# Kernel tuning notes

Hardware: AMD Instinct MI355X
Metric: run time of the kernel (lower is better)

The kernel has to match this reference:

```python
import jax, jax.numpy as jnp
import numpy as np

T, H, I, E, K = 1024, 2048, 1408, 8, 2  # tokens, hidden, moe_intermediate, n_experts, top_k

def setup_inputs() -> dict:
    key = jax.random.key(0)
    k0, k1, k2, k3 = jax.random.split(key, 4)
    def w(k, shape, fan_in):
        return jax.random.normal(k, shape, jnp.float32) / np.float32(np.sqrt(fan_in))
    return {
        "hidden_states": jax.random.normal(k0, (T, H), jnp.float32),
        "gate_w": w(k1, (H, E), H),      # router: LiteLinear(H -> E), no bias
        "w1": w(k2, (E, H, I), H),        # experts_w1 [E, H, I]
        "w2": w(k3, (E, I, H), I),        # experts_w2 [E, I, H]
    }

def reference(hidden_states, gate_w, w1, w2):
    # Router: logits -> softmax -> top-k expert probabilities (no renorm; Qwen2MoE norm_topk_prob=False)
    router_logits = hidden_states @ gate_w                      # [T, E]
    probs = jax.nn.softmax(router_logits, axis=-1)              # [T, E]
    topk_vals, topk_idx = jax.lax.top_k(probs, K)               # [T, K]
    # Dense combine weights: zero except at the top-k experts of each token
    combine = jnp.sum(jax.nn.one_hot(topk_idx, E, dtype=probs.dtype) * topk_vals[..., None], axis=1)  # [T, E]
    # Expert MLP per source: down(silu(x @ w1)) — note: no gate/up split in this repo's fused_moe weights
    h = jnp.einsum('th,ehi->tei', hidden_states, w1)            # [T, E, I]
    y = jnp.einsum('tei,eih->teh', jax.nn.silu(h), w2)          # [T, E, H]
    return jnp.einsum('te,teh->th', combine, y)                 # [T, H]
```

## Files before the change

### kernel.cpp

```cpp
#include <hip/hip_runtime.h>
#include <hip/hip_fp16.h>

#define T_TOK 1024
#define H_DIM 2048
#define I_DIM 1408
#define N_EXP 8
#define TOPK  2

using f16x8 = __attribute__((ext_vector_type(8))) _Float16;
using f32x4 = __attribute__((ext_vector_type(4))) float;

#define BM 64
#define BN 64
#define BK 64
#define NTHR 256
#define MBLKS 32

#define WS_COUNTS      0
#define WS_BASES       256
#define WS_CURSORS     512
#define WS_TOPK_E      768
#define WS_TOPK_W      (768 + 8192)
#define WS_TOK_OF_SLOT 17408
#define WS_W_OF_SLOT   29696
#define WS_HACT        43008
#define WS_NEEDED      (43008 + 8650752)

__global__ void k_router(const float* __restrict__ X, const float* __restrict__ GW,
                         int* __restrict__ counts, int* __restrict__ topk_e,
                         float* __restrict__ topk_w) {
    int t = (blockIdx.x * blockDim.x + threadIdx.x) >> 6;
    int lane = threadIdx.x & 63;
    if (t >= T_TOK) return;
    float acc[N_EXP];
#pragma unroll
    for (int e = 0; e < N_EXP; ++e) acc[e] = 0.f;
    const float* xrow = X + (size_t)t * H_DIM;
    for (int h = lane; h < H_DIM; h += 64) {
        float x = xrow[h];
        const float* g = GW + (size_t)h * N_EXP;
#pragma unroll
        for (int e = 0; e < N_EXP; ++e) acc[e] = fmaf(x, g[e], acc[e]);
    }
#pragma unroll
    for (int off = 32; off > 0; off >>= 1) {
#pragma unroll
        for (int e = 0; e < N_EXP; ++e) acc[e] += __shfl_xor(acc[e], off, 64);
    }
    if (lane == 0) {
        float m = acc[0];
#pragma unroll
        for (int e = 1; e < N_EXP; ++e) m = fmaxf(m, acc[e]);
        float ex[N_EXP], s = 0.f;
#pragma unroll
        for (int e = 0; e < N_EXP; ++e) { ex[e] = expf(acc[e] - m); s += ex[e]; }
        float inv = 1.f / s;
        int e1 = 0;
#pragma unroll
        for (int e = 1; e < N_EXP; ++e) if (ex[e] > ex[e1]) e1 = e;
        int e2 = (e1 == 0) ? 1 : 0;
#pragma unroll
        for (int e = 0; e < N_EXP; ++e) if (e != e1 && ex[e] > ex[e2]) e2 = e;
        topk_e[t * 2 + 0] = e1;
        topk_e[t * 2 + 1] = e2;
        topk_w[t * 2 + 0] = ex[e1] * inv;
        topk_w[t * 2 + 1] = ex[e2] * inv;
        atomicAdd(&counts[e1], 1);
        atomicAdd(&counts[e2], 1);
    }
}

__global__ void k_prefix(const int* __restrict__ counts, int* __restrict__ bases,
                         int* __restrict__ cursors) {
    if (threadIdx.x == 0) {
        int b = 0;
        for (int e = 0; e < N_EXP; ++e) {
            bases[e] = b;
            b += ((counts[e] + BM - 1) / BM) * BM;
            cursors[e] = 0;
        }
    }
}

__global__ void k_scatter(const int* __restrict__ topk_e, const float* __restrict__ topk_w,
                          const int* __restrict__ bases, int* __restrict__ cursors,
                          int* __restrict__ tok_of_slot, float* __restrict__ w_of_slot) {
    int t = blockIdx.x * blockDim.x + threadIdx.x;
    if (t >= T_TOK) return;
    for (int j = 0; j < TOPK; ++j) {
        int e = topk_e[t * 2 + j];
        int pos = atomicAdd(&cursors[e], 1);
        int slot = bases[e] + pos;
        tok_of_slot[slot] = t;
        w_of_slot[slot] = topk_w[t * 2 + j];
    }
}


#define G_COMPUTE(buf)                                                          \
    do {                                                                        \
        _Pragma("unroll") for (int ks = 0; ks < 2; ++ks) {                      \
            f16x8 af[2], bf[2];                                                 \
            _Pragma("unroll") for (int ii = 0; ii < 2; ++ii) {                  \
                int r = wm + ii * 16 + rsel;                                    \
                af[ii] = *(const f16x8*)&As[buf][r][((kq + 4 * ks) ^ (r & 7)) * 8]; \
            }                                                                   \
            _Pragma("unroll") for (int jj = 0; jj < 2; ++jj) {                  \
                int r = wn + jj * 16 + rsel;                                    \
                bf[jj] = *(const f16x8*)&Bs[buf][r][((kq + 4 * ks) ^ (r & 7)) * 8]; \
            }                                                                   \
            _Pragma("unroll") for (int ii = 0; ii < 2; ++ii)                    \
                _Pragma("unroll") for (int jj = 0; jj < 2; ++jj)                \
                    acc[ii][jj] = __builtin_amdgcn_mfma_f32_16x16x32_f16(af[ii], bf[jj], acc[ii][jj], 0, 0, 0); \
        }                                                                       \
    } while (0)

#define G_DECODE(NB)                                \
    const int bi = blockIdx.x;                      \
    const int xcd = bi & 7;                         \
    const int kk = bi >> 3;                         \
    const int mblk = kk & (MBLKS - 1);              \
    const int P = xcd + 8 * (kk >> 5);              \
    const int e = P / (NB);                         \
    const int n = P % (NB);

__global__ __launch_bounds__(NTHR, 3) void k_gemm1(
    const float* __restrict__ X, const float* __restrict__ W1,
    const int* __restrict__ counts, const int* __restrict__ bases,
    const int* __restrict__ tok_of_slot, const float* __restrict__ w_of_slot,
    _Float16* __restrict__ hact) {
    __shared__ _Float16 As[2][BM][BK];
    __shared__ _Float16 Bs[2][BN][BK];

    G_DECODE(I_DIM / BN)
    const int cnt = counts[e];
    const int m0 = mblk * BM;
    if (m0 >= cnt) return;
    const int base = bases[e];
    const int n0 = n * BN;
    const int tid = threadIdx.x;

    const int ar = tid >> 2;
    const int as0 = (tid & 3) * 2;
    const int r_eff = min(ar, cnt - m0 - 1);
    const float* arow = X + (size_t)tok_of_slot[base + m0 + r_eff] * H_DIM + (tid & 3) * 16;

    const int bn = tid & 63;
    const int bc2 = (tid >> 6) * 2;
    const float* bcol = W1 + (size_t)e * (H_DIM * I_DIM) + (size_t)(bc2 * 8) * I_DIM + n0 + bn;

    const int wid = tid >> 6, lane = tid & 63;
    const int wm = (wid >> 1) * 32, wn = (wid & 1) * 32;
    const int rsel = lane & 15, kq = lane >> 4;

    f32x4 acc[2][2] = {};

    float4 aS0[4], aS1[4];
    float  bS0[16], bS1[16];

#define G1_LOAD(aS, bS, k0)                                        \
    do {                                                           \
        const float* ap = arow + (k0);                             \
        aS[0] = *(const float4*)(ap);                              \
        aS[1] = *(const float4*)(ap + 4);                          \
        aS[2] = *(const float4*)(ap + 8);                          \
        aS[3] = *(const float4*)(ap + 12);                         \
        const float* bp = bcol + (size_t)(k0) * I_DIM;             \
        _Pragma("unroll") for (int j = 0; j < 16; ++j)             \
            bS[j] = bp[(size_t)j * I_DIM];                         \
    } while (0)

#define G1_STORE(buf, aS, bS)                                      \
    do {                                                           \
        f16x8 p0, p1;                                              \
        _Pragma("unroll") for (int c = 0; c < 4; ++c) {            \
            p0[c] = (_Float16)aS[0][c]; p0[c + 4] = (_Float16)aS[1][c]; \
            p1[c] = (_Float16)aS[2][c]; p1[c + 4] = (_Float16)aS[3][c]; \
        }                                                          \
        *(f16x8*)&As[buf][ar][((as0) ^ (ar & 7)) * 8] = p0;        \
        *(f16x8*)&As[buf][ar][((as0 + 1) ^ (ar & 7)) * 8] = p1;    \
        f16x8 q0, q1;                                              \
        _Pragma("unroll") for (int j = 0; j < 8; ++j) {            \
            q0[j] = (_Float16)bS[j]; q1[j] = (_Float16)bS[j + 8];  \
        }                                                          \
        *(f16x8*)&Bs[buf][bn][((bc2) ^ (bn & 7)) * 8] = q0;        \
        *(f16x8*)&Bs[buf][bn][((bc2 + 1) ^ (bn & 7)) * 8] = q1;    \
    } while (0)

    constexpr int KT = H_DIM / BK;
    G1_LOAD(aS0, bS0, 0);
    G1_STORE(0, aS0, bS0);
    G1_LOAD(aS0, bS0, BK);
    __syncthreads();
    for (int kt = 0; kt < KT; kt += 2) {
        if (kt + 2 < KT) G1_LOAD(aS1, bS1, (kt + 2) * BK);
        G_COMPUTE(0);
        if (kt + 1 < KT) G1_STORE(1, aS0, bS0);
        __syncthreads();
        if (kt + 3 < KT) G1_LOAD(aS0, bS0, (kt + 3) * BK);
        if (kt + 1 < KT) {
            G_COMPUTE(1);
            if (kt + 2 < KT) G1_STORE(0, aS1, bS1);
            __syncthreads();
        }
    }
#undef G1_LOAD
#undef G1_STORE

    const int rows = cnt - m0;
#pragma unroll
    for (int i = 0; i < 2; ++i) {
#pragma unroll
        for (int rg = 0; rg < 4; ++rg) {
            int r = wm + i * 16 + kq * 4 + rg;
            if (r < rows) {
                int slot = base + m0 + r;
                float w = w_of_slot[slot];
                _Float16* hrow = hact + (size_t)slot * I_DIM + n0;
#pragma unroll
                for (int j = 0; j < 2; ++j) {
                    float v = acc[i][j][rg];
                    hrow[wn + j * 16 + rsel] = (_Float16)(v / (1.f + expf(-v)) * w);
                }
            }
        }
    }
}

__global__ __launch_bounds__(NTHR, 3) void k_gemm2(
    const _Float16* __restrict__ hact, const float* __restrict__ W2,
    const int* __restrict__ counts, const int* __restrict__ bases,
    const int* __restrict__ tok_of_slot, float* __restrict__ out) {
    __shared__ _Float16 As[2][BM][BK];
    __shared__ _Float16 Bs[2][BN][BK];

    G_DECODE(H_DIM / BN)
    const int cnt = counts[e];
    const int m0 = mblk * BM;
    if (m0 >= cnt) return;
    const int base = bases[e];
    const int n0 = n * BN;
    const int tid = threadIdx.x;

    const int ar = tid >> 2;
    const int as0 = (tid & 3) * 2;
    const int r_eff = min(ar, cnt - m0 - 1);
    const _Float16* arow = hact + (size_t)(base + m0 + r_eff) * I_DIM + (tid & 3) * 16;

    const int bn = tid & 63;
    const int bc2 = (tid >> 6) * 2;
    const float* bcol = W2 + (size_t)e * (I_DIM * H_DIM) + (size_t)(bc2 * 8) * H_DIM + n0 + bn;

    const int wid = tid >> 6, lane = tid & 63;
    const int wm = (wid >> 1) * 32, wn = (wid & 1) * 32;
    const int rsel = lane & 15, kq = lane >> 4;

    f32x4 acc[2][2] = {};

    f16x8 aS0[2], aS1[2];
    float bS0[16], bS1[16];

#define G2_LOAD(aS, bS, k0)                                        \
    do {                                                           \
        const _Float16* ap = arow + (k0);                          \
        aS[0] = *(const f16x8*)(ap);                               \
        aS[1] = *(const f16x8*)(ap + 8);                           \
        const float* bp = bcol + (size_t)(k0) * H_DIM;             \
        _Pragma("unroll") for (int j = 0; j < 16; ++j)             \
            bS[j] = bp[(size_t)j * H_DIM];                         \
    } while (0)

#define G2_STORE(buf, aS, bS)                                      \
    do {                                                           \
        *(f16x8*)&As[buf][ar][((as0) ^ (ar & 7)) * 8] = aS[0];     \
        *(f16x8*)&As[buf][ar][((as0 + 1) ^ (ar & 7)) * 8] = aS[1]; \
        f16x8 q0, q1;                                              \
        _Pragma("unroll") for (int j = 0; j < 8; ++j) {            \
            q0[j] = (_Float16)bS[j]; q1[j] = (_Float16)bS[j + 8];  \
        }                                                          \
        *(f16x8*)&Bs[buf][bn][((bc2) ^ (bn & 7)) * 8] = q0;        \
        *(f16x8*)&Bs[buf][bn][((bc2 + 1) ^ (bn & 7)) * 8] = q1;    \
    } while (0)

    constexpr int KT = I_DIM / BK;
    G2_LOAD(aS0, bS0, 0);
    G2_STORE(0, aS0, bS0);
    G2_LOAD(aS0, bS0, BK);
    __syncthreads();
    for (int kt = 0; kt < KT; kt += 2) {
        if (kt + 2 < KT) G2_LOAD(aS1, bS1, (kt + 2) * BK);
        G_COMPUTE(0);
        if (kt + 1 < KT) G2_STORE(1, aS0, bS0);
        __syncthreads();
        if (kt + 3 < KT) G2_LOAD(aS0, bS0, (kt + 3) * BK);
        if (kt + 1 < KT) {
            G_COMPUTE(1);
            if (kt + 2 < KT) G2_STORE(0, aS1, bS1);
            __syncthreads();
        }
    }
#undef G2_LOAD
#undef G2_STORE

    const int rows = cnt - m0;
#pragma unroll
    for (int i = 0; i < 2; ++i) {
#pragma unroll
        for (int rg = 0; rg < 4; ++rg) {
            int r = wm + i * 16 + kq * 4 + rg;
            if (r < rows) {
                int slot = base + m0 + r;
                int tok = tok_of_slot[slot];
                float* orow = out + (size_t)tok * H_DIM + n0;
#pragma unroll
                for (int j = 0; j < 2; ++j)
                    atomicAdd(&orow[wn + j * 16 + rsel], acc[i][j][rg]);
            }
        }
    }
}

extern "C" void kernel_launch(void* const* d_in, const int* in_sizes, int n_in,
                              void* d_out, int out_size, void* d_ws, size_t ws_size,
                              hipStream_t stream) {
    const float* X  = (const float*)d_in[0];
    const float* GW = (const float*)d_in[1];
    const float* W1 = (const float*)d_in[2];
    const float* W2 = (const float*)d_in[3];
    float* out = (float*)d_out;
    char* ws = (char*)d_ws;
    if (ws_size < (size_t)WS_NEEDED) return;

    int*   counts      = (int*)(ws + WS_COUNTS);
    int*   bases       = (int*)(ws + WS_BASES);
    int*   cursors     = (int*)(ws + WS_CURSORS);
    int*   topk_e      = (int*)(ws + WS_TOPK_E);
    float* topk_w      = (float*)(ws + WS_TOPK_W);
    int*   tok_of_slot = (int*)(ws + WS_TOK_OF_SLOT);
    float* w_of_slot   = (float*)(ws + WS_W_OF_SLOT);
    _Float16* hact     = (_Float16*)(ws + WS_HACT);

    hipMemsetAsync(counts, 0, N_EXP * sizeof(int), stream);
    k_router<<<T_TOK / 4, 256, 0, stream>>>(X, GW, counts, topk_e, topk_w);
    k_prefix<<<1, 64, 0, stream>>>(counts, bases, cursors);
    k_scatter<<<T_TOK / 256, 256, 0, stream>>>(topk_e, topk_w, bases, cursors,
                                               tok_of_slot, w_of_slot);
    hipMemsetAsync(out, 0, (size_t)T_TOK * H_DIM * sizeof(float), stream);
    k_gemm1<<<8 * MBLKS * 22, NTHR, 0, stream>>>(
        X, W1, counts, bases, tok_of_slot, w_of_slot, hact);
    k_gemm2<<<8 * MBLKS * 32, NTHR, 0, stream>>>(
        hact, W2, counts, bases, tok_of_slot, out);
}
```

Measured before the change: 184.5 us.

## Deepen global-load register prefetch to four stages in both expert GEMMs

Both expert GEMM kernels now keep four K-tiles of global loads in flight in registers instead of two, rotating through four register buffers while still double-buffering shared memory. Scheduling barriers keep the compiler from interleaving the compute and store phases, and launch bounds drop from 3 to 2 blocks per SM to make room for the extra registers. The aim is to hide the latency of the strided fp32 weight loads, at the cost of lower occupancy and higher register pressure.

```diff
diff --git a/kernel.cpp b/kernel.cpp
--- a/kernel.cpp
+++ b/kernel.cpp
@@ -15,6 +15,8 @@
 #define BK 64
 #define NTHR 256
 #define MBLKS 32
+
+#define SB() __builtin_amdgcn_sched_barrier(0)
 
 #define WS_COUNTS      0
 #define WS_BASES       256
@@ -124,7 +126,7 @@
     const int e = P / (NB);                         \
     const int n = P % (NB);
 
-__global__ __launch_bounds__(NTHR, 3) void k_gemm1(
+__global__ __launch_bounds__(NTHR, 2) void k_gemm1(
     const float* __restrict__ X, const float* __restrict__ W1,
     const int* __restrict__ counts, const int* __restrict__ bases,
     const int* __restrict__ tok_of_slot, const float* __restrict__ w_of_slot,
@@ -155,17 +157,17 @@
 
     f32x4 acc[2][2] = {};
 
-    float4 aS0[4], aS1[4];
-    float  bS0[16], bS1[16];
-
-#define G1_LOAD(aS, bS, k0)                                        \
+    float aS0[16], aS1[16], aS2[16], aS3[16];
+    float bS0[16], bS1[16], bS2[16], bS3[16];
+
+#define G1_LOAD(aS, bS, t)                                         \
     do {                                                           \
-        const float* ap = arow + (k0);                             \
-        aS[0] = *(const float4*)(ap);                              \
-        aS[1] = *(const float4*)(ap + 4);                          \
-        aS[2] = *(const float4*)(ap + 8);                          \
-        aS[3] = *(const float4*)(ap + 12);                         \
-        const float* bp = bcol + (size_t)(k0) * I_DIM;             \
+        const float* ap = arow + (t) * BK;                         \
+        *(float4*)(aS + 0)  = *(const float4*)(ap);                \
+        *(float4*)(aS + 4)  = *(const float4*)(ap + 4);            \
+        *(float4*)(aS + 8)  = *(const float4*)(ap + 8);            \
+        *(float4*)(aS + 12) = *(const float4*)(ap + 12);           \
+        const float* bp = bcol + (size_t)((t) * BK) * I_DIM;       \
         _Pragma("unroll") for (int j = 0; j < 16; ++j)             \
             bS[j] = bp[(size_t)j * I_DIM];                         \
     } while (0)
@@ -173,9 +175,8 @@
 #define G1_STORE(buf, aS, bS)                                      \
     do {                                                           \
         f16x8 p0, p1;                                              \
-        _Pragma("unroll") for (int c = 0; c < 4; ++c) {            \
-            p0[c] = (_Float16)aS[0][c]; p0[c + 4] = (_Float16)aS[1][c]; \
-            p1[c] = (_Float16)aS[2][c]; p1[c + 4] = (_Float16)aS[3][c]; \
+        _Pragma("unroll") for (int c = 0; c < 8; ++c) {            \
+            p0[c] = (_Float16)aS[c]; p1[c] = (_Float16)aS[c + 8];  \
         }                                                          \
         *(f16x8*)&As[buf][ar][((as0) ^ (ar & 7)) * 8] = p0;        \
         *(f16x8*)&As[buf][ar][((as0 + 1) ^ (ar & 7)) * 8] = p1;    \
@@ -188,22 +189,31 @@
     } while (0)
 
     constexpr int KT = H_DIM / BK;
+    constexpr int QUADS = (KT - 1) / 4;
+    constexpr int REM = (KT - 1) & 3;
+
     G1_LOAD(aS0, bS0, 0);
+    G1_LOAD(aS1, bS1, 1);
+    G1_LOAD(aS2, bS2, 2);
+    G1_LOAD(aS3, bS3, 3);
     G1_STORE(0, aS0, bS0);
-    G1_LOAD(aS0, bS0, BK);
     __syncthreads();
-    for (int kt = 0; kt < KT; kt += 2) {
-        if (kt + 2 < KT) G1_LOAD(aS1, bS1, (kt + 2) * BK);
-        G_COMPUTE(0);
-        if (kt + 1 < KT) G1_STORE(1, aS0, bS0);
-        __syncthreads();
-        if (kt + 3 < KT) G1_LOAD(aS0, bS0, (kt + 3) * BK);
-        if (kt + 1 < KT) {
-            G_COMPUTE(1);
-            if (kt + 2 < KT) G1_STORE(0, aS1, bS1);
-            __syncthreads();
-        }
-    }
+
+    int h = 0;
+    for (int q = 0; q < QUADS; ++q, h += 4) {
+        if (h + 4 < KT) G1_LOAD(aS0, bS0, h + 4);
+        SB(); G_COMPUTE(0); SB(); G1_STORE(1, aS1, bS1); __syncthreads();
+        if (h + 5 < KT) G1_LOAD(aS1, bS1, h + 5);
+        SB(); G_COMPUTE(1); SB(); G1_STORE(0, aS2, bS2); __syncthreads();
+        if (h + 6 < KT) G1_LOAD(aS2, bS2, h + 6);
+        SB(); G_COMPUTE(0); SB(); G1_STORE(1, aS3, bS3); __syncthreads();
+        if (h + 7 < KT) G1_LOAD(aS3, bS3, h + 7);
+        SB(); G_COMPUTE(1); SB(); G1_STORE(0, aS0, bS0); __syncthreads();
+    }
+    if constexpr (REM >= 1) { G_COMPUTE(0); G1_STORE(1, aS1, bS1); __syncthreads(); }
+    if constexpr (REM >= 2) { G_COMPUTE(1); G1_STORE(0, aS2, bS2); __syncthreads(); }
+    if constexpr (REM >= 3) { G_COMPUTE(0); G1_STORE(1, aS3, bS3); __syncthreads(); }
+    G_COMPUTE((KT - 1) & 1);
 #undef G1_LOAD
 #undef G1_STORE
 
@@ -227,7 +237,7 @@
     }
 }
 
-__global__ __launch_bounds__(NTHR, 3) void k_gemm2(
+__global__ __launch_bounds__(NTHR, 2) void k_gemm2(
     const _Float16* __restrict__ hact, const float* __restrict__ W2,
     const int* __restrict__ counts, const int* __restrict__ bases,
     const int* __restrict__ tok_of_slot, float* __restrict__ out) {
@@ -257,15 +267,15 @@
 
     f32x4 acc[2][2] = {};
 
-    f16x8 aS0[2], aS1[2];
-    float bS0[16], bS1[16];
-
-#define G2_LOAD(aS, bS, k0)                                        \
+    f16x8 aS0[2], aS1[2], aS2[2], aS3[2];
+    float bS0[16], bS1[16], bS2[16], bS3[16];
+
+#define G2_LOAD(aS, bS, t)                                         \
     do {                                                           \
-        const _Float16* ap = arow + (k0);                          \
+        const _Float16* ap = arow + (t) * BK;                      \
         aS[0] = *(const f16x8*)(ap);                               \
         aS[1] = *(const f16x8*)(ap + 8);                           \
-        const float* bp = bcol + (size_t)(k0) * H_DIM;             \
+        const float* bp = bcol + (size_t)((t) * BK) * H_DIM;       \
         _Pragma("unroll") for (int j = 0; j < 16; ++j)             \
             bS[j] = bp[(size_t)j * H_DIM];                         \
     } while (0)
@@ -283,22 +293,31 @@
     } while (0)
 
     constexpr int KT = I_DIM / BK;
+    constexpr int QUADS = (KT - 1) / 4;
+    constexpr int REM = (KT - 1) & 3;
+
     G2_LOAD(aS0, bS0, 0);
+    G2_LOAD(aS1, bS1, 1);
+    G2_LOAD(aS2, bS2, 2);
+    G2_LOAD(aS3, bS3, 3);
     G2_STORE(0, aS0, bS0);
-    G2_LOAD(aS0, bS0, BK);
     __syncthreads();
-    for (int kt = 0; kt < KT; kt += 2) {
-        if (kt + 2 < KT) G2_LOAD(aS1, bS1, (kt + 2) * BK);
-        G_COMPUTE(0);
-        if (kt + 1 < KT) G2_STORE(1, aS0, bS0);
-        __syncthreads();
-        if (kt + 3 < KT) G2_LOAD(aS0, bS0, (kt + 3) * BK);
-        if (kt + 1 < KT) {
-            G_COMPUTE(1);
-            if (kt + 2 < KT) G2_STORE(0, aS1, bS1);
-            __syncthreads();
-        }
-    }
+
+    int h = 0;
+    for (int q = 0; q < QUADS; ++q, h += 4) {
+        if (h + 4 < KT) G2_LOAD(aS0, bS0, h + 4);
+        SB(); G_COMPUTE(0); SB(); G2_STORE(1, aS1, bS1); __syncthreads();
+        if (h + 5 < KT) G2_LOAD(aS1, bS1, h + 5);
+        SB(); G_COMPUTE(1); SB(); G2_STORE(0, aS2, bS2); __syncthreads();
+        if (h + 6 < KT) G2_LOAD(aS2, bS2, h + 6);
+        SB(); G_COMPUTE(0); SB(); G2_STORE(1, aS3, bS3); __syncthreads();
+        if (h + 7 < KT) G2_LOAD(aS3, bS3, h + 7);
+        SB(); G_COMPUTE(1); SB(); G2_STORE(0, aS0, bS0); __syncthreads();
+    }
+    if constexpr (REM >= 1) { G_COMPUTE(0); G2_STORE(1, aS1, bS1); __syncthreads(); }
+    if constexpr (REM >= 2) { G_COMPUTE(1); G2_STORE(0, aS2, bS2); __syncthreads(); }
+    if constexpr (REM >= 3) { G_COMPUTE(0); G2_STORE(1, aS3, bS3); __syncthreads(); }
+    G_COMPUTE((KT - 1) & 1);
 #undef G2_LOAD
 #undef G2_STORE
 
```

Result: slower. 194.8 us (+5.6%).
